# Optimization experiments

Measured on AMD Instinct MI355X. Metric: run time of the kernel, lower is better.

Reference implementation:

```python
import jax, jax.numpy as jnp
import numpy as np

T, B, H = 512, 128, 512


def setup_inputs() -> dict:
    key = jax.random.key(0)
    k1, k2, k3, k4 = jax.random.split(key, 4)
    scale_i = 1.0 / np.sqrt(H)
    return {
        "ins": jax.random.normal(k1, (T, B, H), dtype=jnp.float32),
        "resets": jax.random.randint(k2, (T, B), 0, 2).astype(bool),
        "h0": jnp.zeros((B, H), dtype=jnp.float32),
        "W_i": jax.random.normal(k3, (H, 3 * H), dtype=jnp.float32) * scale_i,
        "b_i": jnp.zeros((3 * H,), dtype=jnp.float32),
        "W_h": jax.random.normal(k4, (H, 3 * H), dtype=jnp.float32) * scale_i,
        "b_hn": jnp.zeros((H,), dtype=jnp.float32),
    }


def reference(ins, resets, h0, W_i, b_i, W_h, b_hn):
    # Precompute all input-side gate projections in one big GEMM: [T,B,3H]
    gi = jnp.einsum('tbh,hk->tbk', ins, W_i) + b_i

    def step(h, inp):
        gi_t, r_t = inp  # gi_t: [B,3H], r_t: [B] bool
        # episode reset -> zero carry (flax initialize_carry default is zeros)
        h = jnp.where(r_t[:, None], 0.0, h)
        gh = h @ W_h  # [B,3H]
        ir, iz, inn = jnp.split(gi_t, 3, axis=-1)
        hr, hz, hn = jnp.split(gh, 3, axis=-1)
        r = jax.nn.sigmoid(ir + hr)
        z = jax.nn.sigmoid(iz + hz)
        n = jnp.tanh(inn + r * (hn + b_hn))
        new_h = (1.0 - z) * n + z * h
        return new_h, new_h

    final_h, ys = jax.lax.scan(step, h0, (gi, resets))
    return final_h, ys  # carry [B,H], outputs [T,B,H]
```

## Files before the change

### kernel.cpp

```cpp
#include <hip/hip_runtime.h>
#include <stdint.h>
#include <math.h>

#define T_DIM 512
#define B_DIM 128
#define H_DIM 512
#define KSTART_TAIL 3
#define K_MAX_SWEEP 32
#define TOTAL_ROWS (T_DIM * B_DIM)
#define NTG 8

typedef _Float16 half8 __attribute__((ext_vector_type(8)));
typedef float    f32x4 __attribute__((ext_vector_type(4)));

__global__ void k_weights(const float* __restrict__ Wi, const float* __restrict__ Wh,
                          _Float16* __restrict__ Bsw) {
    __shared__ float sh[32][33];
    int nt = blockIdx.x;
    int kt = blockIdx.y;
    int m  = blockIdx.z;
    const float* W = m ? Wh : Wi;
    int ty = threadIdx.x >> 5, tx = threadIdx.x & 31;
    for (int i = 0; i < 4; ++i) {
        int r = ty + i * 8;
        sh[r][tx] = W[(kt * 32 + r) * 1536 + nt * 32 + tx];
    }
    __syncthreads();
    for (int i = 0; i < 4; ++i) {
        int nloc  = ty + i * 8;
        int nglob = nt * 32 + nloc;
        float v   = sh[tx][nloc];
        int kglob = kt * 32 + tx;
        int np, kp;
        if (m == 0) { np = nglob;                                  kp = kglob;       }
        else        { np = (nglob < 1024) ? nglob : nglob + 512;   kp = 512 + kglob; }
        Bsw[np * 1024 + kp] = (_Float16)v;
    }
}

__global__ void k_xcast(const float* __restrict__ ins, _Float16* __restrict__ Acomb) {
    size_t i   = (size_t)blockIdx.x * blockDim.x + threadIdx.x;
    size_t row = i >> 6;
    int    c8  = (int)(i & 63);
    const float4* s = (const float4*)(ins + row * 512 + c8 * 8);
    float4 a = s[0], b = s[1];
    half8 hv;
    hv[0] = (_Float16)a.x; hv[1] = (_Float16)a.y; hv[2] = (_Float16)a.z; hv[3] = (_Float16)a.w;
    hv[4] = (_Float16)b.x; hv[5] = (_Float16)b.y; hv[6] = (_Float16)b.z; hv[7] = (_Float16)b.w;
    *(half8*)(Acomb + row * 1024 + c8 * 8) = hv;
}

__global__ void k_age(const uint8_t* __restrict__ resets, uint16_t* __restrict__ age,
                      int* __restrict__ hist2d) {
    int b = blockIdx.x;
    int t = threadIdx.x;
    __shared__ int sAny;
    __shared__ int sh[512];
    __shared__ int hist[512];
    if (t == 0) sAny = 0;
    hist[t] = 0;
    __syncthreads();
    if ((t & 3) && resets[t]) atomicOr(&sAny, 1);
    __syncthreads();
    bool is_i32 = (sAny == 0);
    int idx = t * B_DIM + b;
    int r;
    if (is_i32) r = (((const int*)resets)[idx] != 0);
    else        r = (resets[idx] != 0);
    sh[t] = r ? t : 0;
    __syncthreads();
    for (int off = 1; off < 512; off <<= 1) {
        int v = (t >= off) ? sh[t - off] : 0;
        __syncthreads();
        if (v > sh[t]) sh[t] = v;
        __syncthreads();
    }
    int a = t - sh[t];
    age[idx] = (uint16_t)a;
    atomicAdd(&hist[a], 1);
    __syncthreads();
    hist2d[b * 512 + t] = hist[t];
}

__global__ void k_prefix(const int* __restrict__ hist2d, int* __restrict__ cnt,
                         int* __restrict__ offs, int* __restrict__ cur,
                         int* __restrict__ bar) {
    int a = threadIdx.x;
    if (a < 160) bar[a] = 0;
    int s = 0;
    for (int b = 0; b < 128; ++b) s += hist2d[b * 512 + a];
    __shared__ int sh[512];
    sh[a] = s;
    __syncthreads();
    for (int off = 1; off < 512; off <<= 1) {
        int v = (a >= off) ? sh[a - off] : 0;
        __syncthreads();
        sh[a] += v;
        __syncthreads();
    }
    cnt[a]  = s;
    offs[a] = sh[a] - s;
    cur[a]  = sh[a] - s;
}

__global__ void k_scatter(const uint16_t* __restrict__ age, int* __restrict__ cur,
                          int* __restrict__ rows) {
    int b = blockIdx.x;
    int t = threadIdx.x;
    __shared__ int lcnt[512];
    __shared__ int lbase[512];
    lcnt[t] = 0;
    __syncthreads();
    int a  = age[t * B_DIM + b];
    int li = atomicAdd(&lcnt[a], 1);
    __syncthreads();
    if (lcnt[t] > 0) lbase[t] = atomicAdd(&cur[t], lcnt[t]);
    __syncthreads();
    rows[lbase[a] + li] = t * B_DIM + b;
}


__launch_bounds__(256, 2)
__global__ void k_gi(const _Float16* __restrict__ AcombC, _Float16* __restrict__ Acomb,
                     const _Float16* __restrict__ Bsw, const uint16_t* __restrict__ age,
                     const float* __restrict__ b_i, const float* __restrict__ b_hn,
                     float* __restrict__ out, _Float16* __restrict__ gi2) {
    int cgi0    = blockIdx.x * 2;
    int rowbase = blockIdx.y * 128;
    float* ys = out + B_DIM * H_DIM;

    __shared__ __align__(16) _Float16 As[128][64];
    __shared__ __align__(16) _Float16 Bs[6][32][64];

    int tid = threadIdx.x;
    f32x4 acc[2][12];
    #pragma unroll
    for (int i = 0; i < 2; ++i)
        #pragma unroll
        for (int j = 0; j < 12; ++j) acc[i][j] = (f32x4){0.f, 0.f, 0.f, 0.f};

    int w = tid >> 6, lane = tid & 63, q = lane >> 4, l15 = lane & 15;
    int w32 = w * 32;
    int lr = tid >> 1, c0 = (tid & 1) * 4, rs = lr & 7;
    int brow = tid >> 3, bch = tid & 7, brs = brow & 7;
    int la = l15 & 7;

    for (int it = 0; it < 8; ++it) {
        int kw = it * 64;
        {
            const uint4* s = (const uint4*)(AcombC + (size_t)(rowbase + lr) * 1024 + kw + c0 * 8);
            uint4 v0 = s[0], v1 = s[1], v2 = s[2], v3 = s[3];
            *(uint4*)&As[lr][((c0 + 0) ^ rs) << 3] = v0;
            *(uint4*)&As[lr][((c0 + 1) ^ rs) << 3] = v1;
            *(uint4*)&As[lr][((c0 + 2) ^ rs) << 3] = v2;
            *(uint4*)&As[lr][((c0 + 3) ^ rs) << 3] = v3;
        }
        {
            #pragma unroll
            for (int s = 0; s < 6; ++s) {
                int c = s / 3, g = s % 3;
                int nb = g * 512 + (cgi0 + c) * 32;
                const uint4* gp = (const uint4*)(Bsw + (size_t)(nb + brow) * 1024 + kw + bch * 8);
                *(uint4*)&Bs[s][brow][(bch ^ brs) << 3] = *gp;
            }
        }
        __syncthreads();
        #pragma unroll
        for (int ks = 0; ks < 2; ++ks) {
            int ca = ks * 4 + q;
            int sc = (ca ^ la) << 3;
            half8 a0 = *(const half8*)&As[w32 + l15][sc];
            half8 a1 = *(const half8*)&As[w32 + 16 + l15][sc];
            #pragma unroll
            for (int s = 0; s < 6; ++s) {
                half8 b0 = *(const half8*)&Bs[s][l15][sc];
                half8 b1 = *(const half8*)&Bs[s][16 + l15][sc];
                acc[0][s*2+0] = __builtin_amdgcn_mfma_f32_16x16x32_f16(a0, b0, acc[0][s*2+0], 0, 0, 0);
                acc[1][s*2+0] = __builtin_amdgcn_mfma_f32_16x16x32_f16(a1, b0, acc[1][s*2+0], 0, 0, 0);
                acc[0][s*2+1] = __builtin_amdgcn_mfma_f32_16x16x32_f16(a0, b1, acc[0][s*2+1], 0, 0, 0);
                acc[1][s*2+1] = __builtin_amdgcn_mfma_f32_16x16x32_f16(a1, b1, acc[1][s*2+1], 0, 0, 0);
            }
        }
        __syncthreads();
    }

    #pragma unroll
    for (int tm = 0; tm < 2; ++tm) {
        #pragma unroll
        for (int reg = 0; reg < 4; ++reg) {
            int lrow = w32 + tm * 16 + q * 4 + reg;
            int row  = rowbase + lrow;
            int t = row >> 7, b = row & 127;
            int a = age[row];
            #pragma unroll
            for (int c = 0; c < 2; ++c) {
                int cgi = cgi0 + c;
                #pragma unroll
                for (int hf = 0; hf < 2; ++hf) {
                    int gj = cgi * 32 + hf * 16 + l15;
                    float rpre = acc[tm][(c*3+0)*2 + hf][reg] + b_i[gj];
                    float zpre = acc[tm][(c*3+1)*2 + hf][reg] + b_i[512 + gj];
                    float innv = acc[tm][(c*3+2)*2 + hf][reg] + b_i[1024 + gj];
                    if (a == 0) {
                        float r = 1.f / (1.f + __expf(-rpre));
                        float z = 1.f / (1.f + __expf(-zpre));
                        float n = tanhf(innv + r * b_hn[gj]);
                        float hnew = (1.f - z) * n;
                        ys[(size_t)row * 512 + gj] = hnew;
                        if (row + 128 < TOTAL_ROWS)
                            Acomb[(size_t)(row + 128) * 1024 + 512 + gj] = (_Float16)hnew;
                        if (t == T_DIM - 1) out[b * 512 + gj] = hnew;
                    } else {
                        size_t gb = ((size_t)cgi * TOTAL_ROWS + row) * 96 + hf * 16 + l15;
                        gi2[gb]      = (_Float16)rpre;
                        gi2[gb + 32] = (_Float16)zpre;
                        gi2[gb + 64] = (_Float16)innv;
                    }
                }
            }
        }
    }
}

__device__ __forceinline__ void sweep_h_tile(
    int cgi, int tileBase, int nrows, int off0,
    _Float16* __restrict__ Acomb, const _Float16* __restrict__ Bsw,
    const int* __restrict__ rows, const _Float16* __restrict__ gi2,
    const float* __restrict__ b_hn, float* __restrict__ out, float* __restrict__ ys,
    int (&rowsL)[128], _Float16 (&As)[128][64], _Float16 (&Bs)[3][32][64])
{
    int tid = threadIdx.x;
    __syncthreads();
    if (tid < 128) {
        int gi = tileBase + tid;
        rowsL[tid] = rows[off0 + ((gi < nrows) ? gi : 0)];
    }
    __syncthreads();

    f32x4 acc[2][6];
    for (int i = 0; i < 2; ++i)
        for (int j = 0; j < 6; ++j) acc[i][j] = (f32x4){0.f, 0.f, 0.f, 0.f};

    int w = tid >> 6, lane = tid & 63, q = lane >> 4, l15 = lane & 15;
    int w32 = w * 32;
    int lr = tid >> 1, c0 = (tid & 1) * 4, rs = lr & 7;
    int brow = tid >> 3, bch = tid & 7, brs = brow & 7;
    int la = l15 & 7;

    for (int it = 0; it < 8; ++it) {
        int kw = it * 64;
        {
            const uint4* s = (const uint4*)(Acomb + (size_t)rowsL[lr] * 1024 + 512 + kw + c0 * 8);
            uint4 v0 = s[0], v1 = s[1], v2 = s[2], v3 = s[3];
            *(uint4*)&As[lr][((c0 + 0) ^ rs) << 3] = v0;
            *(uint4*)&As[lr][((c0 + 1) ^ rs) << 3] = v1;
            *(uint4*)&As[lr][((c0 + 2) ^ rs) << 3] = v2;
            *(uint4*)&As[lr][((c0 + 3) ^ rs) << 3] = v3;
        }
        {
            int nbs[3] = { cgi * 32, 512 + cgi * 32, 1536 + cgi * 32 };
            #pragma unroll
            for (int s = 0; s < 3; ++s) {
                const uint4* g = (const uint4*)(Bsw + (nbs[s] + brow) * 1024 + 512 + kw + bch * 8);
                *(uint4*)&Bs[s][brow][(bch ^ brs) << 3] = *g;
            }
        }
        __syncthreads();
        #pragma unroll
        for (int ks = 0; ks < 2; ++ks) {
            int ca = ks * 4 + q;
            int sc = (ca ^ la) << 3;
            half8 a0 = *(const half8*)&As[w32 + l15][sc];
            half8 a1 = *(const half8*)&As[w32 + 16 + l15][sc];
            #pragma unroll
            for (int s = 0; s < 3; ++s) {
                half8 b0 = *(const half8*)&Bs[s][l15][sc];
                half8 b1 = *(const half8*)&Bs[s][16 + l15][sc];
                acc[0][s*2+0] = __builtin_amdgcn_mfma_f32_16x16x32_f16(a0, b0, acc[0][s*2+0], 0, 0, 0);
                acc[1][s*2+0] = __builtin_amdgcn_mfma_f32_16x16x32_f16(a1, b0, acc[1][s*2+0], 0, 0, 0);
                acc[0][s*2+1] = __builtin_amdgcn_mfma_f32_16x16x32_f16(a0, b1, acc[0][s*2+1], 0, 0, 0);
                acc[1][s*2+1] = __builtin_amdgcn_mfma_f32_16x16x32_f16(a1, b1, acc[1][s*2+1], 0, 0, 0);
            }
        }
        __syncthreads();
    }

    #pragma unroll
    for (int tm = 0; tm < 2; ++tm) {
        #pragma unroll
        for (int reg = 0; reg < 4; ++reg) {
            int lrow = w32 + tm * 16 + q * 4 + reg;
            if (tileBase + lrow >= nrows) continue;
            int row = rowsL[lrow];
            int t = row >> 7, b = row & 127;
            #pragma unroll
            for (int hf = 0; hf < 2; ++hf) {
                int gj = cgi * 32 + hf * 16 + l15;
                size_t gb = ((size_t)cgi * TOTAL_ROWS + row) * 96 + hf * 16 + l15;
                float gr  = (float)gi2[gb];
                float gz  = (float)gi2[gb + 32];
                float gin = (float)gi2[gb + 64];
                float rpre = acc[tm][0 + hf][reg] + gr;
                float zpre = acc[tm][2 + hf][reg] + gz;
                float r = 1.f / (1.f + __expf(-rpre));
                float z = 1.f / (1.f + __expf(-zpre));
                float n = tanhf(gin + r * (acc[tm][4 + hf][reg] + b_hn[gj]));
                float hprev = ys[(size_t)(row - 128) * 512 + gj];
                float hnew  = (1.f - z) * n + z * hprev;
                ys[(size_t)row * 512 + gj] = hnew;
                if (row + 128 < TOTAL_ROWS)
                    Acomb[(size_t)(row + 128) * 1024 + 512 + gj] = (_Float16)hnew;
                if (t == T_DIM - 1) out[b * 512 + gj] = hnew;
            }
        }
    }
}

__launch_bounds__(256, 4)
__global__ void k_sweep_h(_Float16* __restrict__ Acomb, const _Float16* __restrict__ Bsw,
                          const int* __restrict__ rows, const int* __restrict__ cnt,
                          const int* __restrict__ offs, const _Float16* __restrict__ gi2,
                          const float* __restrict__ b_hn, float* __restrict__ out, int sweep) {
    int nrows    = cnt[sweep];
    int tileBase = blockIdx.y * 128;
    if (tileBase >= nrows) return;
    __shared__ int rowsL[128];
    __shared__ __align__(16) _Float16 As[128][64];
    __shared__ __align__(16) _Float16 Bs[3][32][64];
    float* ys = out + B_DIM * H_DIM;
    sweep_h_tile(blockIdx.x, tileBase, nrows, offs[sweep],
                 Acomb, Bsw, rows, gi2, b_hn, out, ys, rowsL, As, Bs);
}

__launch_bounds__(256, 1)
__global__ void k_tail_res(_Float16* __restrict__ Acomb, const _Float16* __restrict__ Bsw,
                           const int* __restrict__ rows, const int* __restrict__ cnt,
                           const int* __restrict__ offs, const _Float16* __restrict__ gi2,
                           const float* __restrict__ b_hn, float* __restrict__ out,
                           int kstart, int* bar) {
    __shared__ __align__(16) _Float16 BsR[3][32][520];
    __shared__ __align__(16) _Float16 As[2][128][64];
    __shared__ int sCnt[512];
    __shared__ int sOffs[512];
    float* ys = out + B_DIM * H_DIM;
    int tid = threadIdx.x;
    int bid = blockIdx.x;
    int cgi = bid & 15, tg = bid >> 4;
    const int nblk = (int)gridDim.x;

    int w = tid >> 6, lane = tid & 63, q = lane >> 4, l15 = lane & 15;
    int w32 = w * 32;
    int lr = tid >> 1, c0 = (tid & 1) * 4, rs = lr & 7;
    int la = l15 & 7;

    {
        int nbs0 = cgi * 32, nbs1 = 512 + cgi * 32, nbs2 = 1536 + cgi * 32;
        #pragma unroll
        for (int i = 0; i < 24; ++i) {
            int idx = tid + i * 256;
            int s   = idx >> 11;
            int rem = idx & 2047;
            int row = rem >> 6;
            int c   = rem & 63;
            int nb  = (s == 0) ? nbs0 : (s == 1) ? nbs1 : nbs2;
            const uint4* g = (const uint4*)(Bsw + (size_t)(nb + row) * 1024 + 512 + c * 8);
            *(uint4*)&BsR[s][row][c * 8] = *g;
        }
        sCnt[tid]        = cnt[tid];
        sCnt[tid + 256]  = cnt[tid + 256];
        sOffs[tid]       = offs[tid];
        sOffs[tid + 256] = offs[tid + 256];
    }
    float bhn0 = b_hn[cgi * 32 + l15];
    float bhn1 = b_hn[cgi * 32 + 16 + l15];
    __syncthreads();

    int phase = 0;

    for (int k = kstart; k < 512; ++k) {
        int done = sOffs[k];
        if (done >= TOTAL_ROWS) break;
        int nrows = sCnt[k];
        int ntiles = (nrows + 127) >> 7;

        for (int ti = tg; ti < ntiles; ti += NTG) {
            int tileBase = ti << 7;

            int er[8];
            #pragma unroll
            for (int e = 0; e < 8; ++e) {
                int tm = e >> 2, reg = e & 3;
                int lrow = w32 + tm * 16 + q * 4 + reg;
                int gidx = tileBase + lrow;
                er[e] = rows[done + ((gidx < nrows) ? gidx : 0)];
            }
            _Float16 pr[8][2], pz[8][2], pi[8][2];
            float    hp[8][2];
            #pragma unroll
            for (int e = 0; e < 8; ++e) {
                #pragma unroll
                for (int hf = 0; hf < 2; ++hf) {
                    int gj = cgi * 32 + hf * 16 + l15;
                    size_t gb = ((size_t)cgi * TOTAL_ROWS + er[e]) * 96 + hf * 16 + l15;
                    pr[e][hf] = gi2[gb];
                    pz[e][hf] = gi2[gb + 32];
                    pi[e][hf] = gi2[gb + 64];
                    hp[e][hf] = ys[(size_t)(er[e] - 128) * 512 + gj];
                }
            }

            int gi0 = tileBase + lr;
            int rowA = rows[done + ((gi0 < nrows) ? gi0 : 0)];
            const _Float16* aSrc = Acomb + (size_t)rowA * 1024 + 512 + c0 * 8;

            f32x4 acc[2][6];
            #pragma unroll
            for (int i = 0; i < 2; ++i)
                #pragma unroll
                for (int j = 0; j < 6; ++j) acc[i][j] = (f32x4){0.f, 0.f, 0.f, 0.f};

            uint4 p0, p1, p2, p3;
            {
                const uint4* s4 = (const uint4*)aSrc;
                p0 = s4[0]; p1 = s4[1]; p2 = s4[2]; p3 = s4[3];
                *(uint4*)&As[0][lr][((c0 + 0) ^ rs) << 3] = p0;
                *(uint4*)&As[0][lr][((c0 + 1) ^ rs) << 3] = p1;
                *(uint4*)&As[0][lr][((c0 + 2) ^ rs) << 3] = p2;
                *(uint4*)&As[0][lr][((c0 + 3) ^ rs) << 3] = p3;
            }

            #pragma unroll
            for (int it = 0; it < 8; ++it) {
                if (it < 7) {
                    const uint4* s4 = (const uint4*)(aSrc + (it + 1) * 64);
                    p0 = s4[0]; p1 = s4[1]; p2 = s4[2]; p3 = s4[3];
                }
                __syncthreads();
                int cur = it & 1;
                #pragma unroll
                for (int ks = 0; ks < 2; ++ks) {
                    int ca  = ks * 4 + q;
                    int sca = (ca ^ la) << 3;
                    int scb = (it * 8 + ca) << 3;
                    half8 a0 = *(const half8*)&As[cur][w32 + l15][sca];
                    half8 a1 = *(const half8*)&As[cur][w32 + 16 + l15][sca];
                    #pragma unroll
                    for (int s = 0; s < 3; ++s) {
                        half8 b0 = *(const half8*)&BsR[s][l15][scb];
                        half8 b1 = *(const half8*)&BsR[s][16 + l15][scb];
                        acc[0][s*2+0] = __builtin_amdgcn_mfma_f32_16x16x32_f16(a0, b0, acc[0][s*2+0], 0, 0, 0);
                        acc[1][s*2+0] = __builtin_amdgcn_mfma_f32_16x16x32_f16(a1, b0, acc[1][s*2+0], 0, 0, 0);
                        acc[0][s*2+1] = __builtin_amdgcn_mfma_f32_16x16x32_f16(a0, b1, acc[0][s*2+1], 0, 0, 0);
                        acc[1][s*2+1] = __builtin_amdgcn_mfma_f32_16x16x32_f16(a1, b1, acc[1][s*2+1], 0, 0, 0);
                    }
                }
                if (it < 7) {
                    int nxt = cur ^ 1;
                    *(uint4*)&As[nxt][lr][((c0 + 0) ^ rs) << 3] = p0;
                    *(uint4*)&As[nxt][lr][((c0 + 1) ^ rs) << 3] = p1;
                    *(uint4*)&As[nxt][lr][((c0 + 2) ^ rs) << 3] = p2;
                    *(uint4*)&As[nxt][lr][((c0 + 3) ^ rs) << 3] = p3;
                }
            }

            #pragma unroll
            for (int e = 0; e < 8; ++e) {
                int tm = e >> 2, reg = e & 3;
                int lrow = w32 + tm * 16 + q * 4 + reg;
                if (tileBase + lrow >= nrows) continue;
                int row = er[e];
                int t = row >> 7, b = row & 127;
                #pragma unroll
                for (int hf = 0; hf < 2; ++hf) {
                    int gj = cgi * 32 + hf * 16 + l15;
                    float rpre = acc[tm][0 + hf][reg] + (float)pr[e][hf];
                    float zpre = acc[tm][2 + hf][reg] + (float)pz[e][hf];
                    float r = 1.f / (1.f + __expf(-rpre));
                    float z = 1.f / (1.f + __expf(-zpre));
                    float n = tanhf((float)pi[e][hf] +
                                    r * (acc[tm][4 + hf][reg] + (hf ? bhn1 : bhn0)));
                    float hnew = (1.f - z) * n + z * hp[e][hf];
                    ys[(size_t)row * 512 + gj] = hnew;
                    if (row + 128 < TOTAL_ROWS)
                        Acomb[(size_t)(row + 128) * 1024 + 512 + gj] = (_Float16)hnew;
                    if (t == T_DIM - 1) out[b * 512 + gj] = hnew;
                }
            }
            __syncthreads();
        }

        ++phase;
        __syncthreads();
        if (tid == 0)
            __hip_atomic_store(&bar[16 + bid], phase, __ATOMIC_RELEASE,
                               __HIP_MEMORY_SCOPE_AGENT);
        if (bid == 0) {
            if (tid < nblk) {
                while (__hip_atomic_load(&bar[16 + tid], __ATOMIC_RELAXED,
                                         __HIP_MEMORY_SCOPE_AGENT) < phase) {
                    __builtin_amdgcn_s_sleep(1);
                }
            }
            __syncthreads();
            if (tid == 0) {
                __builtin_amdgcn_fence(__ATOMIC_ACQUIRE, "agent");
                __hip_atomic_store(&bar[0], phase, __ATOMIC_RELEASE,
                                   __HIP_MEMORY_SCOPE_AGENT);
            }
        }
        if (tid == 0) {
            while (__hip_atomic_load(&bar[0], __ATOMIC_RELAXED,
                                     __HIP_MEMORY_SCOPE_AGENT) < phase) {
                __builtin_amdgcn_s_sleep(1);
            }
            __builtin_amdgcn_fence(__ATOMIC_ACQUIRE, "agent");
        }
        __syncthreads();
    }
}

template <bool F16A>
__launch_bounds__(256, 4)
__global__ void k_sweep(const float* __restrict__ ins, const _Float16* __restrict__ Bsw,
                        _Float16* __restrict__ Acomb, const int* __restrict__ rows,
                        const int* __restrict__ cnt, const int* __restrict__ offs,
                        const float* __restrict__ b_i, const float* __restrict__ b_hn,
                        float* __restrict__ out, int sweep) {
    int nrows    = cnt[sweep];
    int tileBase = blockIdx.y * 128;
    if (tileBase >= nrows) return;
    int cgi  = blockIdx.x;
    int off0 = offs[sweep];
    float* ys = out + B_DIM * H_DIM;

    __shared__ int rowsL[128];
    __shared__ __align__(16) _Float16 As[128][64];
    __shared__ __align__(16) _Float16 Bs[3][32][64];

    int tid = threadIdx.x;
    if (tid < 128) {
        int gi = tileBase + tid;
        rowsL[tid] = rows[off0 + ((gi < nrows) ? gi : 0)];
    }
    __syncthreads();

    f32x4 acc[2][8];
    for (int i = 0; i < 2; ++i)
        for (int j = 0; j < 8; ++j) acc[i][j] = (f32x4){0.f, 0.f, 0.f, 0.f};

    const int kIters = (sweep == 0) ? 8 : 16;
    int w = tid >> 6, lane = tid & 63, q = lane >> 4, l15 = lane & 15;
    int w32 = w * 32;
    int lr = tid >> 1, c0 = (tid & 1) * 4, rs = lr & 7;
    int brow = tid >> 3, bch = tid & 7, brs = brow & 7;
    int la = l15 & 7;

    for (int it = 0; it < kIters; ++it) {
        int  kw    = it * 64;
        bool xpart = (kw < 512);
        if (F16A) {
            const uint4* s = (const uint4*)(Acomb + (size_t)rowsL[lr] * 1024 + kw + c0 * 8);
            uint4 v0 = s[0], v1 = s[1], v2 = s[2], v3 = s[3];
            *(uint4*)&As[lr][((c0 + 0) ^ rs) << 3] = v0;
            *(uint4*)&As[lr][((c0 + 1) ^ rs) << 3] = v1;
            *(uint4*)&As[lr][((c0 + 2) ^ rs) << 3] = v2;
            *(uint4*)&As[lr][((c0 + 3) ^ rs) << 3] = v3;
        } else {
            int rowidx = rowsL[lr];
            const float* src = xpart ? (ins + (size_t)rowidx * 512 + kw)
                                     : (ys + (size_t)(rowidx - 128) * 512 + (kw - 512));
            const float4* s4 = (const float4*)(src + c0 * 8);
            float4 v[8];
            #pragma unroll
            for (int j = 0; j < 8; ++j) v[j] = s4[j];
            #pragma unroll
            for (int c = 0; c < 4; ++c) {
                float4 a = v[c * 2], b2 = v[c * 2 + 1];
                half8 hv;
                hv[0] = (_Float16)a.x;  hv[1] = (_Float16)a.y;
                hv[2] = (_Float16)a.z;  hv[3] = (_Float16)a.w;
                hv[4] = (_Float16)b2.x; hv[5] = (_Float16)b2.y;
                hv[6] = (_Float16)b2.z; hv[7] = (_Float16)b2.w;
                *(half8*)&As[lr][((c0 + c) ^ rs) << 3] = hv;
            }
        }
        {
            int nbs[3];
            nbs[0] = cgi * 32;
            nbs[1] = 512 + cgi * 32;
            nbs[2] = (xpart ? 1024 : 1536) + cgi * 32;
            #pragma unroll
            for (int s = 0; s < 3; ++s) {
                const uint4* g = (const uint4*)(Bsw + (nbs[s] + brow) * 1024 + kw + bch * 8);
                *(uint4*)&Bs[s][brow][(bch ^ brs) << 3] = *g;
            }
        }
        __syncthreads();
        #pragma unroll
        for (int ks = 0; ks < 2; ++ks) {
            int ca = ks * 4 + q;
            int sc = (ca ^ la) << 3;
            half8 a0  = *(const half8*)&As[w32 + l15][sc];
            half8 a1  = *(const half8*)&As[w32 + 16 + l15][sc];
            half8 b00 = *(const half8*)&Bs[0][l15][sc];
            half8 b01 = *(const half8*)&Bs[0][16 + l15][sc];
            half8 b10 = *(const half8*)&Bs[1][l15][sc];
            half8 b11 = *(const half8*)&Bs[1][16 + l15][sc];
            half8 b20 = *(const half8*)&Bs[2][l15][sc];
            half8 b21 = *(const half8*)&Bs[2][16 + l15][sc];
            acc[0][0] = __builtin_amdgcn_mfma_f32_16x16x32_f16(a0, b00, acc[0][0], 0, 0, 0);
            acc[1][0] = __builtin_amdgcn_mfma_f32_16x16x32_f16(a1, b00, acc[1][0], 0, 0, 0);
            acc[0][1] = __builtin_amdgcn_mfma_f32_16x16x32_f16(a0, b01, acc[0][1], 0, 0, 0);
            acc[1][1] = __builtin_amdgcn_mfma_f32_16x16x32_f16(a1, b01, acc[1][1], 0, 0, 0);
            acc[0][2] = __builtin_amdgcn_mfma_f32_16x16x32_f16(a0, b10, acc[0][2], 0, 0, 0);
            acc[1][2] = __builtin_amdgcn_mfma_f32_16x16x32_f16(a1, b10, acc[1][2], 0, 0, 0);
            acc[0][3] = __builtin_amdgcn_mfma_f32_16x16x32_f16(a0, b11, acc[0][3], 0, 0, 0);
            acc[1][3] = __builtin_amdgcn_mfma_f32_16x16x32_f16(a1, b11, acc[1][3], 0, 0, 0);
            if (xpart) {
                acc[0][4] = __builtin_amdgcn_mfma_f32_16x16x32_f16(a0, b20, acc[0][4], 0, 0, 0);
                acc[1][4] = __builtin_amdgcn_mfma_f32_16x16x32_f16(a1, b20, acc[1][4], 0, 0, 0);
                acc[0][5] = __builtin_amdgcn_mfma_f32_16x16x32_f16(a0, b21, acc[0][5], 0, 0, 0);
                acc[1][5] = __builtin_amdgcn_mfma_f32_16x16x32_f16(a1, b21, acc[1][5], 0, 0, 0);
            } else {
                acc[0][6] = __builtin_amdgcn_mfma_f32_16x16x32_f16(a0, b20, acc[0][6], 0, 0, 0);
                acc[1][6] = __builtin_amdgcn_mfma_f32_16x16x32_f16(a1, b20, acc[1][6], 0, 0, 0);
                acc[0][7] = __builtin_amdgcn_mfma_f32_16x16x32_f16(a0, b21, acc[0][7], 0, 0, 0);
                acc[1][7] = __builtin_amdgcn_mfma_f32_16x16x32_f16(a1, b21, acc[1][7], 0, 0, 0);
            }
        }
        __syncthreads();
    }

    #pragma unroll
    for (int tm = 0; tm < 2; ++tm) {
        int lrow_base = w32 + tm * 16 + q * 4;
        #pragma unroll
        for (int reg = 0; reg < 4; ++reg) {
            int lrow = lrow_base + reg;
            if (tileBase + lrow >= nrows) continue;
            int rowidx = rowsL[lrow];
            int t = rowidx >> 7, b = rowidx & 127;
            #pragma unroll
            for (int hf = 0; hf < 2; ++hf) {
                int gj = cgi * 32 + hf * 16 + l15;
                float rpre = acc[tm][0 + hf][reg] + b_i[gj];
                float zpre = acc[tm][2 + hf][reg] + b_i[512 + gj];
                float innv = acc[tm][4 + hf][reg] + b_i[1024 + gj];
                float hnv  = acc[tm][6 + hf][reg];
                float r = 1.f / (1.f + __expf(-rpre));
                float z = 1.f / (1.f + __expf(-zpre));
                float n = tanhf(innv + r * (hnv + b_hn[gj]));
                float hprev = (sweep > 0) ? ys[(size_t)(rowidx - 128) * 512 + gj] : 0.f;
                float hnew  = (1.f - z) * n + z * hprev;
                ys[(size_t)rowidx * 512 + gj] = hnew;
                if (F16A && rowidx + 128 < TOTAL_ROWS)
                    Acomb[(size_t)(rowidx + 128) * 1024 + 512 + gj] = (_Float16)hnew;
                if (t == T_DIM - 1) out[b * 512 + gj] = hnew;
            }
        }
    }
}

__global__ void k_cleanup(const float* __restrict__ ins, const _Float16* __restrict__ Bsw,
                          const int* __restrict__ rows, const int* __restrict__ cnt,
                          const int* __restrict__ offs, const float* __restrict__ b_i,
                          const float* __restrict__ b_hn, float* __restrict__ out) {
    float* ys = out + B_DIM * H_DIM;
    __shared__ float xs[512], hs[512];
    int j = threadIdx.x;
    for (int a = K_MAX_SWEEP; a < 512; ++a) {
        int n = cnt[a];
        if (n == 0) return;
        int o = offs[a];
        for (int i = 0; i < n; ++i) {
            int rowidx = rows[o + i];
            xs[j] = ins[rowidx * 512 + j];
            hs[j] = ys[(rowidx - 128) * 512 + j];
            __syncthreads();
            float rpre = b_i[j], zpre = b_i[512 + j], innv = b_i[1024 + j], hnv = 0.f;
            for (int k = 0; k < 512; ++k) {
                float xk = xs[k], hk = hs[k];
                rpre += xk * (float)Bsw[j * 1024 + k]          + hk * (float)Bsw[j * 1024 + 512 + k];
                zpre += xk * (float)Bsw[(512 + j) * 1024 + k]  + hk * (float)Bsw[(512 + j) * 1024 + 512 + k];
                innv += xk * (float)Bsw[(1024 + j) * 1024 + k];
                hnv  += hk * (float)Bsw[(1536 + j) * 1024 + 512 + k];
            }
            float r  = 1.f / (1.f + __expf(-rpre));
            float z  = 1.f / (1.f + __expf(-zpre));
            float nn = tanhf(innv + r * (hnv + b_hn[j]));
            float hnew = (1.f - z) * nn + z * hs[j];
            ys[rowidx * 512 + j] = hnew;
            int t = rowidx >> 7, b = rowidx & 127;
            if (t == 511) out[b * 512 + j] = hnew;
            __syncthreads();
        }
    }
}

extern "C" void kernel_launch(void* const* d_in, const int* in_sizes, int n_in,
                              void* d_out, int out_size, void* d_ws, size_t ws_size,
                              hipStream_t stream) {
    const float*   ins    = (const float*)d_in[0];
    const uint8_t* resets = (const uint8_t*)d_in[1];
    const float*   Wi     = (const float*)d_in[3];
    const float*   b_i    = (const float*)d_in[4];
    const float*   Wh     = (const float*)d_in[5];
    const float*   b_hn   = (const float*)d_in[6];
    float*         out    = (float*)d_out;

    const size_t BSW_B   = 2048ull * 1024 * 2;
    const size_t ACOMB_B = 65536ull * 1024 * 2;
    const size_t GI2_B   = 16ull * TOTAL_ROWS * 96 * 2;
    const size_t FIXED_B = 131072 + 262144 + 3 * 2048 + 262144 + 1024;

    char* ws = (char*)d_ws;
    size_t off = 0;
    _Float16* Bsw    = (_Float16*)(ws + off); off += BSW_B;
    uint16_t* age    = (uint16_t*)(ws + off); off += 131072;
    int*      hist2d = (int*)(ws + off);      off += 262144;
    int*      cnt    = (int*)(ws + off);      off += 2048;
    int*      offs   = (int*)(ws + off);      off += 2048;
    int*      cur    = (int*)(ws + off);      off += 2048;
    int*      rows   = (int*)(ws + off);      off += 262144;
    int*      bar    = (int*)(ws + off);      off += 1024;

    bool big      = (ws_size >= BSW_B + FIXED_B + ACOMB_B);
    bool new_path = (ws_size >= BSW_B + FIXED_B + ACOMB_B + GI2_B);
    _Float16* Acomb = nullptr;
    _Float16* gi2   = nullptr;
    if (big)      { Acomb = (_Float16*)(ws + off); off += ACOMB_B; }
    if (new_path) { gi2   = (_Float16*)(ws + off); off += GI2_B;   }

    k_weights<<<dim3(48, 16, 2), dim3(256), 0, stream>>>(Wi, Wh, Bsw);
    if (big)
        k_xcast<<<dim3(16384), dim3(256), 0, stream>>>(ins, Acomb);
    k_age    <<<dim3(128), dim3(512), 0, stream>>>(resets, age, hist2d);
    k_prefix <<<dim3(1),   dim3(512), 0, stream>>>(hist2d, cnt, offs, cur, bar);
    k_scatter<<<dim3(128), dim3(512), 0, stream>>>(age, cur, rows);

    if (new_path) {
        k_gi<<<dim3(8, 512), dim3(256), 0, stream>>>(Acomb, Acomb, Bsw, age, b_i, b_hn, out, gi2);
        for (int k = 1; k < KSTART_TAIL; ++k) {
            int tiles = 512 / (k + 1) + 1;
            k_sweep_h<<<dim3(16, tiles), dim3(256), 0, stream>>>(Acomb, Bsw, rows, cnt, offs,
                                                                 gi2, b_hn, out, k);
        }
        k_tail_res<<<dim3(128), dim3(256), 0, stream>>>(Acomb, Bsw, rows, cnt, offs,
                                                        gi2, b_hn, out, KSTART_TAIL, bar);
    } else {
        for (int k = 0; k < K_MAX_SWEEP; ++k) {
            int tiles = 512 / (k + 1) + 1;
            if (tiles > 512) tiles = 512;
            if (big)
                k_sweep<true><<<dim3(16, tiles), dim3(256), 0, stream>>>(ins, Bsw, Acomb, rows,
                                                                         cnt, offs, b_i, b_hn, out, k);
            else
                k_sweep<false><<<dim3(16, tiles), dim3(256), 0, stream>>>(ins, Bsw, Acomb, rows,
                                                                          cnt, offs, b_i, b_hn, out, k);
        }
        k_cleanup<<<dim3(1), dim3(512), 0, stream>>>(ins, Bsw, rows, cnt, offs, b_i, b_hn, out);
    }
}
```

Measured before the change: 911.5 us.

## Restrict input-gate GEMM to tail rows and use fused sweeps for early ages

The input-side gate GEMM kernel now gathers only rows whose reset age is at least the tail start, instead of computing gi for every row and writing fp16 gi2 for all nonzero-age rows. Ages 0 to 2 are handled by the existing fused k_sweep kernel, which computes both input and hidden projections per age level. This reduces the gi2 write traffic and GEMM work spent on early-age rows. In exchange the early sweeps redo a full-K input GEMM with gathered row loads, and the old dedicated h-only sweep kernel is removed.

Measured after the change: 791.0 us. 13.2% less time.

```diff
diff --git a/kernel.cpp b/kernel.cpp
--- a/kernel.cpp
+++ b/kernel.cpp
@@ -119,20 +119,28 @@
     rows[lbase[a] + li] = t * B_DIM + b;
 }
 
-
 __launch_bounds__(256, 2)
-__global__ void k_gi(const _Float16* __restrict__ AcombC, _Float16* __restrict__ Acomb,
-                     const _Float16* __restrict__ Bsw, const uint16_t* __restrict__ age,
-                     const float* __restrict__ b_i, const float* __restrict__ b_hn,
-                     float* __restrict__ out, _Float16* __restrict__ gi2) {
-    int cgi0    = blockIdx.x * 2;
-    int rowbase = blockIdx.y * 128;
-    float* ys = out + B_DIM * H_DIM;
-
+__global__ void k_gi_g(const _Float16* __restrict__ AcombC, const _Float16* __restrict__ Bsw,
+                       const int* __restrict__ rows, const int* __restrict__ offs,
+                       const float* __restrict__ b_i, _Float16* __restrict__ gi2,
+                       int kstart) {
+    int off3  = offs[kstart];
+    int nrows = TOTAL_ROWS - off3;
+    int tileBase = blockIdx.y * 128;
+    if (tileBase >= nrows) return;
+    int cgi0 = blockIdx.x * 2;
+
+    __shared__ int rowsL[128];
     __shared__ __align__(16) _Float16 As[128][64];
     __shared__ __align__(16) _Float16 Bs[6][32][64];
 
     int tid = threadIdx.x;
+    if (tid < 128) {
+        int gi = tileBase + tid;
+        rowsL[tid] = rows[off3 + ((gi < nrows) ? gi : 0)];
+    }
+    __syncthreads();
+
     f32x4 acc[2][12];
     #pragma unroll
     for (int i = 0; i < 2; ++i)
@@ -148,7 +156,7 @@
     for (int it = 0; it < 8; ++it) {
         int kw = it * 64;
         {
-            const uint4* s = (const uint4*)(AcombC + (size_t)(rowbase + lr) * 1024 + kw + c0 * 8);
+            const uint4* s = (const uint4*)(AcombC + (size_t)rowsL[lr] * 1024 + kw + c0 * 8);
             uint4 v0 = s[0], v1 = s[1], v2 = s[2], v3 = s[3];
             *(uint4*)&As[lr][((c0 + 0) ^ rs) << 3] = v0;
             *(uint4*)&As[lr][((c0 + 1) ^ rs) << 3] = v1;
@@ -189,9 +197,8 @@
         #pragma unroll
         for (int reg = 0; reg < 4; ++reg) {
             int lrow = w32 + tm * 16 + q * 4 + reg;
-            int row  = rowbase + lrow;
-            int t = row >> 7, b = row & 127;
-            int a = age[row];
+            if (tileBase + lrow >= nrows) continue;
+            int row = rowsL[lrow];
             #pragma unroll
             for (int c = 0; c < 2; ++c) {
                 int cgi = cgi0 + c;
@@ -201,135 +208,14 @@
                     float rpre = acc[tm][(c*3+0)*2 + hf][reg] + b_i[gj];
                     float zpre = acc[tm][(c*3+1)*2 + hf][reg] + b_i[512 + gj];
                     float innv = acc[tm][(c*3+2)*2 + hf][reg] + b_i[1024 + gj];
-                    if (a == 0) {
-                        float r = 1.f / (1.f + __expf(-rpre));
-                        float z = 1.f / (1.f + __expf(-zpre));
-                        float n = tanhf(innv + r * b_hn[gj]);
-                        float hnew = (1.f - z) * n;
-                        ys[(size_t)row * 512 + gj] = hnew;
-                        if (row + 128 < TOTAL_ROWS)
-                            Acomb[(size_t)(row + 128) * 1024 + 512 + gj] = (_Float16)hnew;
-                        if (t == T_DIM - 1) out[b * 512 + gj] = hnew;
-                    } else {
-                        size_t gb = ((size_t)cgi * TOTAL_ROWS + row) * 96 + hf * 16 + l15;
-                        gi2[gb]      = (_Float16)rpre;
-                        gi2[gb + 32] = (_Float16)zpre;
-                        gi2[gb + 64] = (_Float16)innv;
-                    }
+                    size_t gb = ((size_t)cgi * TOTAL_ROWS + row) * 96 + hf * 16 + l15;
+                    gi2[gb]      = (_Float16)rpre;
+                    gi2[gb + 32] = (_Float16)zpre;
+                    gi2[gb + 64] = (_Float16)innv;
                 }
             }
         }
     }
-}
-
-__device__ __forceinline__ void sweep_h_tile(
-    int cgi, int tileBase, int nrows, int off0,
-    _Float16* __restrict__ Acomb, const _Float16* __restrict__ Bsw,
-    const int* __restrict__ rows, const _Float16* __restrict__ gi2,
-    const float* __restrict__ b_hn, float* __restrict__ out, float* __restrict__ ys,
-    int (&rowsL)[128], _Float16 (&As)[128][64], _Float16 (&Bs)[3][32][64])
-{
-    int tid = threadIdx.x;
-    __syncthreads();
-    if (tid < 128) {
-        int gi = tileBase + tid;
-        rowsL[tid] = rows[off0 + ((gi < nrows) ? gi : 0)];
-    }
-    __syncthreads();
-
-    f32x4 acc[2][6];
-    for (int i = 0; i < 2; ++i)
-        for (int j = 0; j < 6; ++j) acc[i][j] = (f32x4){0.f, 0.f, 0.f, 0.f};
-
-    int w = tid >> 6, lane = tid & 63, q = lane >> 4, l15 = lane & 15;
-    int w32 = w * 32;
-    int lr = tid >> 1, c0 = (tid & 1) * 4, rs = lr & 7;
-    int brow = tid >> 3, bch = tid & 7, brs = brow & 7;
-    int la = l15 & 7;
-
-    for (int it = 0; it < 8; ++it) {
-        int kw = it * 64;
-        {
-            const uint4* s = (const uint4*)(Acomb + (size_t)rowsL[lr] * 1024 + 512 + kw + c0 * 8);
-            uint4 v0 = s[0], v1 = s[1], v2 = s[2], v3 = s[3];
-            *(uint4*)&As[lr][((c0 + 0) ^ rs) << 3] = v0;
-            *(uint4*)&As[lr][((c0 + 1) ^ rs) << 3] = v1;
-            *(uint4*)&As[lr][((c0 + 2) ^ rs) << 3] = v2;
-            *(uint4*)&As[lr][((c0 + 3) ^ rs) << 3] = v3;
-        }
-        {
-            int nbs[3] = { cgi * 32, 512 + cgi * 32, 1536 + cgi * 32 };
-            #pragma unroll
-            for (int s = 0; s < 3; ++s) {
-                const uint4* g = (const uint4*)(Bsw + (nbs[s] + brow) * 1024 + 512 + kw + bch * 8);
-                *(uint4*)&Bs[s][brow][(bch ^ brs) << 3] = *g;
-            }
-        }
-        __syncthreads();
-        #pragma unroll
-        for (int ks = 0; ks < 2; ++ks) {
-            int ca = ks * 4 + q;
-            int sc = (ca ^ la) << 3;
-            half8 a0 = *(const half8*)&As[w32 + l15][sc];
-            half8 a1 = *(const half8*)&As[w32 + 16 + l15][sc];
-            #pragma unroll
-            for (int s = 0; s < 3; ++s) {
-                half8 b0 = *(const half8*)&Bs[s][l15][sc];
-                half8 b1 = *(const half8*)&Bs[s][16 + l15][sc];
-                acc[0][s*2+0] = __builtin_amdgcn_mfma_f32_16x16x32_f16(a0, b0, acc[0][s*2+0], 0, 0, 0);
-                acc[1][s*2+0] = __builtin_amdgcn_mfma_f32_16x16x32_f16(a1, b0, acc[1][s*2+0], 0, 0, 0);
-                acc[0][s*2+1] = __builtin_amdgcn_mfma_f32_16x16x32_f16(a0, b1, acc[0][s*2+1], 0, 0, 0);
-                acc[1][s*2+1] = __builtin_amdgcn_mfma_f32_16x16x32_f16(a1, b1, acc[1][s*2+1], 0, 0, 0);
-            }
-        }
-        __syncthreads();
-    }
-
-    #pragma unroll
-    for (int tm = 0; tm < 2; ++tm) {
-        #pragma unroll
-        for (int reg = 0; reg < 4; ++reg) {
-            int lrow = w32 + tm * 16 + q * 4 + reg;
-            if (tileBase + lrow >= nrows) continue;
-            int row = rowsL[lrow];
-            int t = row >> 7, b = row & 127;
-            #pragma unroll
-            for (int hf = 0; hf < 2; ++hf) {
-                int gj = cgi * 32 + hf * 16 + l15;
-                size_t gb = ((size_t)cgi * TOTAL_ROWS + row) * 96 + hf * 16 + l15;
-                float gr  = (float)gi2[gb];
-                float gz  = (float)gi2[gb + 32];
-                float gin = (float)gi2[gb + 64];
-                float rpre = acc[tm][0 + hf][reg] + gr;
-                float zpre = acc[tm][2 + hf][reg] + gz;
-                float r = 1.f / (1.f + __expf(-rpre));
-                float z = 1.f / (1.f + __expf(-zpre));
-                float n = tanhf(gin + r * (acc[tm][4 + hf][reg] + b_hn[gj]));
-                float hprev = ys[(size_t)(row - 128) * 512 + gj];
-                float hnew  = (1.f - z) * n + z * hprev;
-                ys[(size_t)row * 512 + gj] = hnew;
-                if (row + 128 < TOTAL_ROWS)
-                    Acomb[(size_t)(row + 128) * 1024 + 512 + gj] = (_Float16)hnew;
-                if (t == T_DIM - 1) out[b * 512 + gj] = hnew;
-            }
-        }
-    }
-}
-
-__launch_bounds__(256, 4)
-__global__ void k_sweep_h(_Float16* __restrict__ Acomb, const _Float16* __restrict__ Bsw,
-                          const int* __restrict__ rows, const int* __restrict__ cnt,
-                          const int* __restrict__ offs, const _Float16* __restrict__ gi2,
-                          const float* __restrict__ b_hn, float* __restrict__ out, int sweep) {
-    int nrows    = cnt[sweep];
-    int tileBase = blockIdx.y * 128;
-    if (tileBase >= nrows) return;
-    __shared__ int rowsL[128];
-    __shared__ __align__(16) _Float16 As[128][64];
-    __shared__ __align__(16) _Float16 Bs[3][32][64];
-    float* ys = out + B_DIM * H_DIM;
-    sweep_h_tile(blockIdx.x, tileBase, nrows, offs[sweep],
-                 Acomb, Bsw, rows, gi2, b_hn, out, ys, rowsL, As, Bs);
 }
 
 __launch_bounds__(256, 1)
@@ -739,11 +625,13 @@
     k_scatter<<<dim3(128), dim3(512), 0, stream>>>(age, cur, rows);
 
     if (new_path) {
-        k_gi<<<dim3(8, 512), dim3(256), 0, stream>>>(Acomb, Acomb, Bsw, age, b_i, b_hn, out, gi2);
-        for (int k = 1; k < KSTART_TAIL; ++k) {
+        k_gi_g<<<dim3(8, 512), dim3(256), 0, stream>>>(Acomb, Bsw, rows, offs, b_i, gi2,
+                                                       KSTART_TAIL);
+        for (int k = 0; k < KSTART_TAIL; ++k) {
             int tiles = 512 / (k + 1) + 1;
-            k_sweep_h<<<dim3(16, tiles), dim3(256), 0, stream>>>(Acomb, Bsw, rows, cnt, offs,
-                                                                 gi2, b_hn, out, k);
+            if (tiles > 512) tiles = 512;
+            k_sweep<true><<<dim3(16, tiles), dim3(256), 0, stream>>>(ins, Bsw, Acomb, rows,
+                                                                     cnt, offs, b_i, b_hn, out, k);
         }
         k_tail_res<<<dim3(128), dim3(256), 0, stream>>>(Acomb, Bsw, rows, cnt, offs,
                                                         gi2, b_hn, out, KSTART_TAIL, bar);
```
